# Optimization experiments

Hardware: AMD Instinct MI355X
Metric: run time of the kernel (lower is better)

## Reference

```python
import jax, jax.numpy as jnp
import numpy as np

B, S, D = 32, 1, 2048
H, KVH, HD = 16, 4, 128
MAXS = 4096
EPS = 1e-5
NREP = H // KVH  # GQA repeat factor = 4
FF = 4 * D
POS = 4095  # decode position (start_pos)


def setup_inputs() -> dict:
    key = jax.random.key(0)
    ks = jax.random.split(key, 12)
    sc = lambda d: 1.0 / np.sqrt(d)
    # RoPE angles for the current token position, [S, HD//2]
    inv_freq = 1.0 / (10000.0 ** (np.arange(0, HD, 2, dtype=np.float32) / HD))
    ang = (POS + np.arange(S, dtype=np.float32))[:, None] * inv_freq[None, :]
    return {
        "x": jax.random.normal(ks[0], (B, S, D), jnp.float32),
        "cos": jnp.asarray(np.cos(ang), jnp.float32),
        "sin": jnp.asarray(np.sin(ang), jnp.float32),
        "k_cache": jax.random.normal(ks[1], (B, MAXS, KVH, HD), jnp.float32),
        "v_cache": jax.random.normal(ks[2], (B, MAXS, KVH, HD), jnp.float32),
        "w_rms_attn": jnp.ones((D,), jnp.float32),
        "wq": jax.random.normal(ks[3], (D, D), jnp.float32) * sc(D),
        "wk": jax.random.normal(ks[4], (D, KVH * HD), jnp.float32) * sc(D),
        "wv": jax.random.normal(ks[5], (D, KVH * HD), jnp.float32) * sc(D),
        "wo": jax.random.normal(ks[6], (D, D), jnp.float32) * sc(D),
        "w_rms_ffn": jnp.ones((D,), jnp.float32),
        "w1": jax.random.normal(ks[7], (D, FF), jnp.float32) * sc(D),
        "w2": jax.random.normal(ks[8], (D, FF), jnp.float32) * sc(D),
        "w3": jax.random.normal(ks[9], (FF, D), jnp.float32) * sc(FF),
        "start_pos": POS,
    }


def _rmsnorm(x, g):
    return x * g * jax.lax.rsqrt(jnp.mean(x * x, axis=-1, keepdims=True) + EPS)


def _rope(x, cos, sin):
    # x: [B, S, h, HD]; complex rotation on (even, odd) pairs
    xr = x.reshape(*x.shape[:-1], HD // 2, 2)
    x0, x1 = xr[..., 0], xr[..., 1]
    c = cos[None, :, None, :]
    s = sin[None, :, None, :]
    r0 = x0 * c - x1 * s
    r1 = x0 * s + x1 * c
    return jnp.stack([r0, r1], axis=-1).reshape(x.shape)


def reference(x, cos, sin, k_cache, v_cache, w_rms_attn, wq, wk, wv, wo,
              w_rms_ffn, w1, w2, w3, start_pos):
    xa = _rmsnorm(x, w_rms_attn)
    xq = (xa @ wq).reshape(B, S, H, HD)
    xk = (xa @ wk).reshape(B, S, KVH, HD)
    xv = (xa @ wv).reshape(B, S, KVH, HD)
    # Source applies RoPE to K and V (not Q) -- reproduced faithfully.
    xk = _rope(xk, cos, sin)
    xv = _rope(xv, cos, sin)
    kc = jax.lax.dynamic_update_slice(k_cache, xk, (0, start_pos, 0, 0))
    vc = jax.lax.dynamic_update_slice(v_cache, xv, (0, start_pos, 0, 0))
    klen = start_pos + S
    keys = jnp.repeat(kc[:, :klen], NREP, axis=2)   # [B, klen, H, HD]
    vals = jnp.repeat(vc[:, :klen], NREP, axis=2)
    att = jnp.einsum('bqhd,bkhd->bhqk', xq, keys) * (HD ** -0.5)
    att = jax.nn.softmax(att, axis=-1)
    y = jnp.einsum('bhqk,bkhd->bqhd', att, vals).reshape(B, S, D)
    h = x + y @ wo
    xf = _rmsnorm(h, w_rms_ffn)
    return h + (jax.nn.silu(xf @ w1) * (xf @ w2)) @ w3
```

## Files before the change

kernel.cpp:

```cpp
#include <hip/hip_runtime.h>
#include <math.h>

#define BB 32
#define DD 2048
#define NKVH 4
#define HDIM 128
#define MAXS 4096
#define FFD 8192
#define POS 4095
#define EPSV 1e-5f
#define SCALE 0.08838834764831845f
#define ASPLIT 32
#define SPOS 128

#define OFF_QT   0u
#define OFF_KT   65536u
#define OFF_VT   81920u
#define OFF_G1   98304u
#define OFF_G2   360448u
#define ZERO_N   622592u
#define OFF_XAT  622592u
#define OFF_RK   688128u
#define OFF_RV   704512u
#define OFF_PML  720896u
#define OFF_PACC 753664u
#define OFF_YT   2850816u
#define OFF_H    2916352u
#define OFF_XFT  2981888u
#define OFF_KFIX 3047424u
#define OFF_VFIX 3309568u

#define VM_WAIT8 asm volatile("s_waitcnt vmcnt(8)" ::: "memory")
#define VM_WAIT0 asm volatile("s_waitcnt vmcnt(0)" ::: "memory")
#define LG_WAIT0 asm volatile("s_waitcnt lgkmcnt(0)" ::: "memory")
#define SCHED0   __builtin_amdgcn_sched_barrier(0)
#define SBAR     __builtin_amdgcn_s_barrier()

#define REP32(M) M(0) M(1) M(2) M(3) M(4) M(5) M(6) M(7) M(8) M(9) M(10) M(11) M(12) M(13) M(14) M(15) M(16) M(17) M(18) M(19) M(20) M(21) M(22) M(23) M(24) M(25) M(26) M(27) M(28) M(29) M(30) M(31)
#define REP32A(M,X) M(0,X) M(1,X) M(2,X) M(3,X) M(4,X) M(5,X) M(6,X) M(7,X) M(8,X) M(9,X) M(10,X) M(11,X) M(12,X) M(13,X) M(14,X) M(15,X) M(16,X) M(17,X) M(18,X) M(19,X) M(20,X) M(21,X) M(22,X) M(23,X) M(24,X) M(25,X) M(26,X) M(27,X) M(28,X) M(29,X) M(30,X) M(31,X)

#define DECLA(i) float a##i = 0.f;
#define FMA1(i,k) a##i = fmaf(ap[(k)*32 + (i)], w##k, a##i);
#define STORET(i) tl[i] = a##i;
#define ATOMN(i) atomicAdd(C + (size_t)(i)*N + n, a##i);

template<int N, int CH, bool TOUT>
__device__ __forceinline__ void gemv_body(const float* __restrict__ At,
                                          const float* __restrict__ W,
                                          float* __restrict__ C, int colblk,
                                          float* tile) {
    int tid = (int)threadIdx.x;
    int n = colblk * 256 + tid;
    int d0 = blockIdx.y * CH;
    const float* Wp = W + (size_t)d0 * N + n;
    const float* ap = At + (size_t)d0 * 32;
    REP32(DECLA)
#pragma unroll 4
    for (int dd = 0; dd < CH; dd += 4) {
        float w0 = Wp[0];
        float w1 = Wp[(size_t)N];
        float w2 = Wp[(size_t)N * 2];
        float w3 = Wp[(size_t)N * 3];
        REP32A(FMA1, 0)
        REP32A(FMA1, 1)
        REP32A(FMA1, 2)
        REP32A(FMA1, 3)
        Wp += (size_t)N * 4;
        ap += 128;
    }
    if constexpr (TOUT) {
        float* tl = tile + tid * 33;
        REP32(STORET)
        __syncthreads();
        float* cb = C + (size_t)colblk * 256 * 32;
#pragma unroll
        for (int i = 0; i < 32; ++i) {
            int f = i * 256 + tid;
            atomicAdd(cb + f, tile[(f >> 5) * 33 + (f & 31)]);
        }
    } else {
        REP32(ATOMN)
    }
}

template<int N, int CH, bool TOUT>
__global__ __launch_bounds__(256) void gemv32_kernel(const float* __restrict__ At,
                                                     const float* __restrict__ W,
                                                     float* __restrict__ C) {
    if constexpr (TOUT) {
        __shared__ float tile[256 * 33];
        gemv_body<N, CH, true>(At, W, C, blockIdx.x, tile);
    } else {
        gemv_body<N, CH, false>(At, W, C, blockIdx.x, nullptr);
    }
}

template<int N, int CH, int HALF>
__global__ __launch_bounds__(256) void gemv32_dual_kernel(const float* __restrict__ At,
        const float* __restrict__ W0, const float* __restrict__ W1,
        float* __restrict__ C0, float* __restrict__ C1) {
    __shared__ float tile[256 * 33];
    int bx = blockIdx.x;
    if (bx < HALF) gemv_body<N, CH, true>(At, W0, C0, bx, tile);
    else           gemv_body<N, CH, true>(At, W1, C1, bx - HALF, tile);
}

__global__ void zero_kernel(float* __restrict__ p) {
    p[blockIdx.x * 256 + threadIdx.x] = 0.f;
}

__global__ void rmsnorm_kernel(const float* __restrict__ in, const float* __restrict__ g,
                               float* __restrict__ outT, float* __restrict__ cpy) {
    int b = blockIdx.x;
    int tid = threadIdx.x;
    const float* row = in + b * DD;
    float v[8];
    float ss = 0.f;
#pragma unroll
    for (int i = 0; i < 8; ++i) { v[i] = row[tid + i * 256]; ss += v[i] * v[i]; }
#pragma unroll
    for (int off = 32; off; off >>= 1) ss += __shfl_xor(ss, off);
    __shared__ float red[4];
    if ((tid & 63) == 0) red[tid >> 6] = ss;
    __syncthreads();
    ss = red[0] + red[1] + red[2] + red[3];
    float scale = rsqrtf(ss * (1.f / DD) + EPSV);
#pragma unroll
    for (int i = 0; i < 8; ++i) {
        int idx = tid + i * 256;
        outT[(size_t)idx * 32 + b] = v[i] * g[idx] * scale;
        if (cpy) cpy[b * DD + idx] = v[i];
    }
}

__global__ void rope_kernel(const float* __restrict__ kT, const float* __restrict__ vT,
                            const float* __restrict__ cosb, const float* __restrict__ sinb,
                            float* __restrict__ rk, float* __restrict__ rv) {
    int idx = blockIdx.x * 256 + threadIdx.x;
    int b = idx >> 8, rem = idx & 255;
    int kvh = rem >> 6, i = rem & 63;
    float c = cosb[i], s = sinb[i];
    int col = kvh * HDIM + 2 * i;
    float k0 = kT[(size_t)col * 32 + b], k1 = kT[(size_t)(col + 1) * 32 + b];
    float v0 = vT[(size_t)col * 32 + b], v1 = vT[(size_t)(col + 1) * 32 + b];
    int o = (b * NKVH + kvh) * HDIM + 2 * i;
    rk[o] = k0 * c - k1 * s; rk[o + 1] = k0 * s + k1 * c;
    rv[o] = v0 * c - v1 * s; rv[o + 1] = v0 * s + v1 * c;
}

__global__ void fixlast_kernel(const float* __restrict__ kc, const float* __restrict__ vc,
                               const float* __restrict__ rk, const float* __restrict__ rv,
                               float* __restrict__ kfix, float* __restrict__ vfix) {
    int idx = blockIdx.x * 256 + threadIdx.x;
    int b = idx >> 13, rem = idx & 8191;
    int pos = rem >> 9, col = rem & 511;
    int gpos = 4080 + pos;
    float kv, vv;
    if (gpos == POS) {
        kv = rk[b * 512 + col]; vv = rv[b * 512 + col];
    } else {
        size_t o = ((size_t)(b * MAXS + gpos)) * 512 + col;
        kv = kc[o]; vv = vc[o];
    }
    kfix[idx] = kv; vfix[idx] = vv;
}

__global__ __launch_bounds__(256, 2) void attn_stage_kernel(
    const float* __restrict__ qn, const float* __restrict__ kc, const float* __restrict__ vc,
    const float* __restrict__ kfix, const float* __restrict__ vfix,
    float* __restrict__ pml, float* __restrict__ pacc) {
    int split = blockIdx.x & 31, b = blockIdx.x >> 5;
    int tid = threadIdx.x, lane = tid & 63, wv = tid >> 6;
    __shared__ float kbuf[2][8192];
    __shared__ float p_s[128][16];
    int qpos = tid >> 4, qhead = tid & 15;
    int qr = qpos * 4 + (qhead >> 2);
    int vh = tid >> 4, c16 = tid & 15, vkvh = vh >> 2;
    int t0 = split * SPOS;

    float4 qrot[32];
#pragma unroll
    for (int j = 0; j < 32; ++j) {
        int g = (j + qr) & 31;
        qrot[j] = *(const float4*)(qn + (size_t)b * DD + qhead * HDIM + g * 4);
    }
    float4 av0 = {0, 0, 0, 0}, av1 = {0, 0, 0, 0};

    auto stage = [&](int t) {
        int s = t & 7;
        const float* base;
        if (t < 8) base = (split == 31 && s == 7) ? kfix + (size_t)b * 8192
                                                  : kc + ((size_t)b * MAXS + t0 + s * 16) * 512;
        else       base = (split == 31 && s == 7) ? vfix + (size_t)b * 8192
                                                  : vc + ((size_t)b * MAXS + t0 + s * 16) * 512;
        const float* g = base + wv * 2048 + lane * 4;
        float* l = &kbuf[t & 1][wv * 2048];
#pragma unroll
        for (int i = 0; i < 8; ++i)
            __builtin_amdgcn_global_load_lds(
                (const __attribute__((address_space(1))) void*)(g + i * 256),
                (__attribute__((address_space(3))) void*)(l + i * 256), 16, 0, 0);
    };

    stage(0);
    for (int t = 0; t < 16; ++t) {
        if (t < 15) { stage(t + 1); VM_WAIT8; } else { VM_WAIT0; }
        SCHED0; SBAR;
        if (t == 8) {
#pragma unroll
            for (int hh = 0; hh < 4; ++hh) {
                int h = wv * 4 + hh;
                float e0 = p_s[lane][h], e1 = p_s[lane + 64][h];
                float m = fmaxf(e0, e1);
#pragma unroll
                for (int off = 32; off; off >>= 1) m = fmaxf(m, __shfl_xor(m, off));
                e0 = __expf(e0 - m); e1 = __expf(e1 - m);
                p_s[lane][h] = e0; p_s[lane + 64][h] = e1;
                float l2 = e0 + e1;
#pragma unroll
                for (int off = 32; off; off >>= 1) l2 += __shfl_xor(l2, off);
                if (lane == 0) {
                    int idx = ((b * ASPLIT + split) * 16 + h) * 2;
                    pml[idx] = m; pml[idx + 1] = l2;
                }
            }
        }
        const float* kb = kbuf[t & 1];
        if (t < 8) {
            float4 acc = {0, 0, 0, 0};
            const float* rowp = kb + qr * 128;
#pragma unroll
            for (int j = 0; j < 32; ++j) {
                int g = (j + qr) & 31;
                float4 k4 = *(const float4*)(rowp + g * 4);
                acc.x = fmaf(k4.x, qrot[j].x, acc.x);
                acc.y = fmaf(k4.y, qrot[j].y, acc.y);
                acc.z = fmaf(k4.z, qrot[j].z, acc.z);
                acc.w = fmaf(k4.w, qrot[j].w, acc.w);
            }
            p_s[t * 16 + qpos][qhead] = (acc.x + acc.y + acc.z + acc.w) * SCALE;
        } else {
            int s = t - 8;
            const float* vrow = kb + vkvh * 128 + c16 * 4;
#pragma unroll
            for (int p = 0; p < 16; ++p) {
                float pw = p_s[s * 16 + p][vh];
                float4 v0 = *(const float4*)(vrow + p * 512);
                float4 v1 = *(const float4*)(vrow + p * 512 + 64);
                av0.x = fmaf(pw, v0.x, av0.x); av0.y = fmaf(pw, v0.y, av0.y);
                av0.z = fmaf(pw, v0.z, av0.z); av0.w = fmaf(pw, v0.w, av0.w);
                av1.x = fmaf(pw, v1.x, av1.x); av1.y = fmaf(pw, v1.y, av1.y);
                av1.z = fmaf(pw, v1.z, av1.z); av1.w = fmaf(pw, v1.w, av1.w);
            }
        }
        LG_WAIT0; SCHED0; SBAR;
    }
    size_t pbase = ((size_t)(b * ASPLIT + split) * 16 + vh) * HDIM;
    *(float4*)(pacc + pbase + c16 * 4) = av0;
    *(float4*)(pacc + pbase + 64 + c16 * 4) = av1;
}

__global__ void attn_combine_kernel(const float* __restrict__ pml,
                                    const float* __restrict__ pacc, float* __restrict__ yT) {
    int bid = blockIdx.x;
    int b = bid >> 4, h = bid & 15;
    int d = threadIdx.x;
    float M = -INFINITY;
#pragma unroll 8
    for (int s = 0; s < ASPLIT; ++s)
        M = fmaxf(M, pml[((b * ASPLIT + s) * 16 + h) * 2]);
    float denom = 0.f, acc = 0.f;
#pragma unroll 4
    for (int s = 0; s < ASPLIT; ++s) {
        int idx = (b * ASPLIT + s) * 16 + h;
        float e = __expf(pml[idx * 2] - M);
        denom += pml[idx * 2 + 1] * e;
        acc += e * pacc[(size_t)idx * HDIM + d];
    }
    yT[(size_t)(h * HDIM + d) * 32 + b] = acc / denom;
}

__global__ void silu_mul_kernel(float* __restrict__ g1, const float* __restrict__ g2) {
    int i = blockIdx.x * 256 + threadIdx.x;
    float a = g1[i], bb = g2[i];
    g1[i] = a * bb / (1.f + __expf(-a));
}

extern "C" void kernel_launch(void* const* d_in, const int* in_sizes, int n_in,
                              void* d_out, int out_size, void* d_ws, size_t ws_size,
                              hipStream_t stream) {
    (void)in_sizes; (void)n_in; (void)out_size; (void)ws_size;
    const float* x    = (const float*)d_in[0];
    const float* cosb = (const float*)d_in[1];
    const float* sinb = (const float*)d_in[2];
    const float* kc   = (const float*)d_in[3];
    const float* vc   = (const float*)d_in[4];
    const float* wra  = (const float*)d_in[5];
    const float* wq   = (const float*)d_in[6];
    const float* wk   = (const float*)d_in[7];
    const float* wv   = (const float*)d_in[8];
    const float* wo   = (const float*)d_in[9];
    const float* wrf  = (const float*)d_in[10];
    const float* w1   = (const float*)d_in[11];
    const float* w2   = (const float*)d_in[12];
    const float* w3   = (const float*)d_in[13];
    float* out = (float*)d_out;
    float* ws  = (float*)d_ws;

    float* qn   = ws + OFF_QT;
    float* kT   = ws + OFF_KT;
    float* vT   = ws + OFF_VT;
    float* g1T  = ws + OFF_G1;
    float* g2T  = ws + OFF_G2;
    float* xaT  = ws + OFF_XAT;
    float* rk   = ws + OFF_RK;
    float* rv   = ws + OFF_RV;
    float* pml  = ws + OFF_PML;
    float* pacc = ws + OFF_PACC;
    float* yT   = ws + OFF_YT;
    float* h    = ws + OFF_H;
    float* xfT  = ws + OFF_XFT;
    float* kfix = ws + OFF_KFIX;
    float* vfix = ws + OFF_VFIX;

    zero_kernel<<<ZERO_N / 256, 256, 0, stream>>>(ws);

    rmsnorm_kernel<<<32, 256, 0, stream>>>(x, wra, xaT, h);
    gemv32_kernel<2048, 32, false><<<dim3(8, 64), 256, 0, stream>>>(xaT, wq, qn);
    gemv32_dual_kernel<512, 32, 2><<<dim3(4, 64), 256, 0, stream>>>(xaT, wk, wv, kT, vT);
    rope_kernel<<<32, 256, 0, stream>>>(kT, vT, cosb, sinb, rk, rv);
    fixlast_kernel<<<1024, 256, 0, stream>>>(kc, vc, rk, rv, kfix, vfix);
    attn_stage_kernel<<<1024, 256, 0, stream>>>(qn, kc, vc, kfix, vfix, pml, pacc);
    attn_combine_kernel<<<512, 128, 0, stream>>>(pml, pacc, yT);
    gemv32_kernel<2048, 32, false><<<dim3(8, 64), 256, 0, stream>>>(yT, wo, h);
    rmsnorm_kernel<<<32, 256, 0, stream>>>(h, wrf, xfT, out);
    gemv32_dual_kernel<8192, 128, 32><<<dim3(64, 16), 256, 0, stream>>>(xfT, w1, w2, g1T, g2T);
    silu_mul_kernel<<<1024, 256, 0, stream>>>(g1T, g2T);
    gemv32_kernel<2048, 128, false><<<dim3(8, 64), 256, 0, stream>>>(g1T, w3, out);
}
```

Measured before the change: 309.7 us.

## Make attention waves independent with per-wave buffers and fuse RoPE into fixlast

The attention stage kernel now gives each wavefront its own 32-position slice and its own double-buffered LDS region. Each wave computes a local softmax max and sum, so the block-wide barriers inside the 16-step loop are gone. The four waves' partial results are merged once at the end through LDS with rescaling. The RoPE kernel is folded into the fixlast kernel, which removes one launch and the rk/rv intermediates. The cost is more accumulator registers per thread (8 float4) and an extra intra-block reduction at the end.

Result: no change. 304.2 us (-1.8%).

```diff
diff --git a/kernel.cpp b/kernel.cpp
--- a/kernel.cpp
+++ b/kernel.cpp
@@ -20,8 +20,6 @@
 #define OFF_G2   360448u
 #define ZERO_N   622592u
 #define OFF_XAT  622592u
-#define OFF_RK   688128u
-#define OFF_RV   704512u
 #define OFF_PML  720896u
 #define OFF_PACC 753664u
 #define OFF_YT   2850816u
@@ -30,11 +28,9 @@
 #define OFF_KFIX 3047424u
 #define OFF_VFIX 3309568u
 
-#define VM_WAIT8 asm volatile("s_waitcnt vmcnt(8)" ::: "memory")
-#define VM_WAIT0 asm volatile("s_waitcnt vmcnt(0)" ::: "memory")
-#define LG_WAIT0 asm volatile("s_waitcnt lgkmcnt(0)" ::: "memory")
-#define SCHED0   __builtin_amdgcn_sched_barrier(0)
-#define SBAR     __builtin_amdgcn_s_barrier()
+#define VM_WAIT8  asm volatile("s_waitcnt vmcnt(8)" ::: "memory")
+#define VM_WAIT0  asm volatile("s_waitcnt vmcnt(0)" ::: "memory")
+#define SCHED0    __builtin_amdgcn_sched_barrier(0)
 
 #define REP32(M) M(0) M(1) M(2) M(3) M(4) M(5) M(6) M(7) M(8) M(9) M(10) M(11) M(12) M(13) M(14) M(15) M(16) M(17) M(18) M(19) M(20) M(21) M(22) M(23) M(24) M(25) M(26) M(27) M(28) M(29) M(30) M(31)
 #define REP32A(M,X) M(0,X) M(1,X) M(2,X) M(3,X) M(4,X) M(5,X) M(6,X) M(7,X) M(8,X) M(9,X) M(10,X) M(11,X) M(12,X) M(13,X) M(14,X) M(15,X) M(16,X) M(17,X) M(18,X) M(19,X) M(20,X) M(21,X) M(22,X) M(23,X) M(24,X) M(25,X) M(26,X) M(27,X) M(28,X) M(29,X) M(30,X) M(31,X)
@@ -133,23 +129,9 @@
     }
 }
 
-__global__ void rope_kernel(const float* __restrict__ kT, const float* __restrict__ vT,
-                            const float* __restrict__ cosb, const float* __restrict__ sinb,
-                            float* __restrict__ rk, float* __restrict__ rv) {
-    int idx = blockIdx.x * 256 + threadIdx.x;
-    int b = idx >> 8, rem = idx & 255;
-    int kvh = rem >> 6, i = rem & 63;
-    float c = cosb[i], s = sinb[i];
-    int col = kvh * HDIM + 2 * i;
-    float k0 = kT[(size_t)col * 32 + b], k1 = kT[(size_t)(col + 1) * 32 + b];
-    float v0 = vT[(size_t)col * 32 + b], v1 = vT[(size_t)(col + 1) * 32 + b];
-    int o = (b * NKVH + kvh) * HDIM + 2 * i;
-    rk[o] = k0 * c - k1 * s; rk[o + 1] = k0 * s + k1 * c;
-    rv[o] = v0 * c - v1 * s; rv[o + 1] = v0 * s + v1 * c;
-}
-
-__global__ void fixlast_kernel(const float* __restrict__ kc, const float* __restrict__ vc,
-                               const float* __restrict__ rk, const float* __restrict__ rv,
+__global__ void fixrope_kernel(const float* __restrict__ kc, const float* __restrict__ vc,
+                               const float* __restrict__ kT, const float* __restrict__ vT,
+                               const float* __restrict__ cosb, const float* __restrict__ sinb,
                                float* __restrict__ kfix, float* __restrict__ vfix) {
     int idx = blockIdx.x * 256 + threadIdx.x;
     int b = idx >> 13, rem = idx & 8191;
@@ -157,7 +139,13 @@
     int gpos = 4080 + pos;
     float kv, vv;
     if (gpos == POS) {
-        kv = rk[b * 512 + col]; vv = rv[b * 512 + col];
+        int d = col & 127, i = d >> 1;
+        float c = cosb[i], s = sinb[i];
+        int colp = col & ~1;
+        float k0 = kT[(size_t)colp * 32 + b], k1 = kT[(size_t)(colp + 1) * 32 + b];
+        float v0 = vT[(size_t)colp * 32 + b], v1 = vT[(size_t)(colp + 1) * 32 + b];
+        if (d & 1) { kv = k0 * s + k1 * c; vv = v0 * s + v1 * c; }
+        else       { kv = k0 * c - k1 * s; vv = v0 * c - v1 * s; }
     } else {
         size_t o = ((size_t)(b * MAXS + gpos)) * 512 + col;
         kv = kc[o]; vv = vc[o];
@@ -165,18 +153,20 @@
     kfix[idx] = kv; vfix[idx] = vv;
 }
 
-__global__ __launch_bounds__(256, 2) void attn_stage_kernel(
+__global__ __launch_bounds__(256, 2) void attn_wave_kernel(
     const float* __restrict__ qn, const float* __restrict__ kc, const float* __restrict__ vc,
     const float* __restrict__ kfix, const float* __restrict__ vfix,
     float* __restrict__ pml, float* __restrict__ pacc) {
     int split = blockIdx.x & 31, b = blockIdx.x >> 5;
-    int tid = threadIdx.x, lane = tid & 63, wv = tid >> 6;
-    __shared__ float kbuf[2][8192];
+    int tid = threadIdx.x, w = tid >> 6, lane = tid & 63;
+    __shared__ float kbuf[4][2][2048];
     __shared__ float p_s[128][16];
-    int qpos = tid >> 4, qhead = tid & 15;
-    int qr = qpos * 4 + (qhead >> 2);
-    int vh = tid >> 4, c16 = tid & 15, vkvh = vh >> 2;
+    __shared__ float m_s[4][16], l_s[4][16];
+    int qpos = lane >> 4, qhead = lane & 15;
+    int qr = lane >> 2;
+    int c16 = lane & 15, vh0 = lane >> 4;
     int t0 = split * SPOS;
+    int wbase = w * 32;
 
     float4 qrot[32];
 #pragma unroll
@@ -184,17 +174,21 @@
         int g = (j + qr) & 31;
         qrot[j] = *(const float4*)(qn + (size_t)b * DD + qhead * HDIM + g * 4);
     }
-    float4 av0 = {0, 0, 0, 0}, av1 = {0, 0, 0, 0};
-
-    auto stage = [&](int t) {
-        int s = t & 7;
+    float4 a[8];
+#pragma unroll
+    for (int k = 0; k < 8; ++k) a[k] = (float4){0, 0, 0, 0};
+
+    auto stage = [&](int s) {
+        int sk = s & 7;
+        int g0 = t0 + wbase + sk * 4;
+        bool fix = (split == 31) && (w == 3) && (sk >= 4);
         const float* base;
-        if (t < 8) base = (split == 31 && s == 7) ? kfix + (size_t)b * 8192
-                                                  : kc + ((size_t)b * MAXS + t0 + s * 16) * 512;
-        else       base = (split == 31 && s == 7) ? vfix + (size_t)b * 8192
-                                                  : vc + ((size_t)b * MAXS + t0 + s * 16) * 512;
-        const float* g = base + wv * 2048 + lane * 4;
-        float* l = &kbuf[t & 1][wv * 2048];
+        if (s < 8) base = fix ? kfix + (size_t)b * 8192 + (sk - 4) * 2048
+                              : kc + ((size_t)b * MAXS + g0) * 512;
+        else       base = fix ? vfix + (size_t)b * 8192 + (sk - 4) * 2048
+                              : vc + ((size_t)b * MAXS + g0) * 512;
+        const float* g = base + lane * 4;
+        float* l = &kbuf[w][s & 1][0];
 #pragma unroll
         for (int i = 0; i < 8; ++i)
             __builtin_amdgcn_global_load_lds(
@@ -203,29 +197,11 @@
     };
 
     stage(0);
+#pragma unroll 1
     for (int t = 0; t < 16; ++t) {
         if (t < 15) { stage(t + 1); VM_WAIT8; } else { VM_WAIT0; }
-        SCHED0; SBAR;
-        if (t == 8) {
-#pragma unroll
-            for (int hh = 0; hh < 4; ++hh) {
-                int h = wv * 4 + hh;
-                float e0 = p_s[lane][h], e1 = p_s[lane + 64][h];
-                float m = fmaxf(e0, e1);
-#pragma unroll
-                for (int off = 32; off; off >>= 1) m = fmaxf(m, __shfl_xor(m, off));
-                e0 = __expf(e0 - m); e1 = __expf(e1 - m);
-                p_s[lane][h] = e0; p_s[lane + 64][h] = e1;
-                float l2 = e0 + e1;
-#pragma unroll
-                for (int off = 32; off; off >>= 1) l2 += __shfl_xor(l2, off);
-                if (lane == 0) {
-                    int idx = ((b * ASPLIT + split) * 16 + h) * 2;
-                    pml[idx] = m; pml[idx + 1] = l2;
-                }
-            }
-        }
-        const float* kb = kbuf[t & 1];
+        SCHED0;
+        const float* kb = &kbuf[w][t & 1][0];
         if (t < 8) {
             float4 acc = {0, 0, 0, 0};
             const float* rowp = kb + qr * 128;
@@ -238,26 +214,96 @@
                 acc.z = fmaf(k4.z, qrot[j].z, acc.z);
                 acc.w = fmaf(k4.w, qrot[j].w, acc.w);
             }
-            p_s[t * 16 + qpos][qhead] = (acc.x + acc.y + acc.z + acc.w) * SCALE;
+            p_s[wbase + t * 4 + qpos][qhead] = (acc.x + acc.y + acc.z + acc.w) * SCALE;
+            if (t == 7) {
+                int h = lane >> 2, sub = lane & 3;
+                float v[8];
+                float m = -INFINITY;
+#pragma unroll
+                for (int j = 0; j < 8; ++j) {
+                    v[j] = p_s[wbase + sub * 8 + j][h];
+                    m = fmaxf(m, v[j]);
+                }
+                m = fmaxf(m, __shfl_xor(m, 1));
+                m = fmaxf(m, __shfl_xor(m, 2));
+                float lsum = 0.f;
+#pragma unroll
+                for (int j = 0; j < 8; ++j) {
+                    float e = __expf(v[j] - m);
+                    p_s[wbase + sub * 8 + j][h] = e;
+                    lsum += e;
+                }
+                lsum += __shfl_xor(lsum, 1);
+                lsum += __shfl_xor(lsum, 2);
+                if (sub == 0) { m_s[w][h] = m; l_s[w][h] = lsum; }
+            }
         } else {
             int s = t - 8;
-            const float* vrow = kb + vkvh * 128 + c16 * 4;
-#pragma unroll
-            for (int p = 0; p < 16; ++p) {
-                float pw = p_s[s * 16 + p][vh];
-                float4 v0 = *(const float4*)(vrow + p * 512);
-                float4 v1 = *(const float4*)(vrow + p * 512 + 64);
-                av0.x = fmaf(pw, v0.x, av0.x); av0.y = fmaf(pw, v0.y, av0.y);
-                av0.z = fmaf(pw, v0.z, av0.z); av0.w = fmaf(pw, v0.w, av0.w);
-                av1.x = fmaf(pw, v1.x, av1.x); av1.y = fmaf(pw, v1.y, av1.y);
-                av1.z = fmaf(pw, v1.z, av1.z); av1.w = fmaf(pw, v1.w, av1.w);
+#pragma unroll
+            for (int j = 0; j < 4; ++j) {
+#pragma unroll
+                for (int p = 0; p < 4; ++p) {
+                    float pw = p_s[wbase + s * 4 + p][vh0 + 4 * j];
+                    const float* vr = kb + p * 512 + j * 128 + c16 * 4;
+                    float4 v0 = *(const float4*)(vr);
+                    float4 v1 = *(const float4*)(vr + 64);
+                    a[j * 2].x = fmaf(pw, v0.x, a[j * 2].x);
+                    a[j * 2].y = fmaf(pw, v0.y, a[j * 2].y);
+                    a[j * 2].z = fmaf(pw, v0.z, a[j * 2].z);
+                    a[j * 2].w = fmaf(pw, v0.w, a[j * 2].w);
+                    a[j * 2 + 1].x = fmaf(pw, v1.x, a[j * 2 + 1].x);
+                    a[j * 2 + 1].y = fmaf(pw, v1.y, a[j * 2 + 1].y);
+                    a[j * 2 + 1].z = fmaf(pw, v1.z, a[j * 2 + 1].z);
+                    a[j * 2 + 1].w = fmaf(pw, v1.w, a[j * 2 + 1].w);
+                }
             }
         }
-        LG_WAIT0; SCHED0; SBAR;
-    }
-    size_t pbase = ((size_t)(b * ASPLIT + split) * 16 + vh) * HDIM;
-    *(float4*)(pacc + pbase + c16 * 4) = av0;
-    *(float4*)(pacc + pbase + 64 + c16 * 4) = av1;
+    }
+    __syncthreads();
+    float fac[4];
+#pragma unroll
+    for (int j = 0; j < 4; ++j) {
+        int h = vh0 + 4 * j;
+        float M = fmaxf(fmaxf(m_s[0][h], m_s[1][h]), fmaxf(m_s[2][h], m_s[3][h]));
+        fac[j] = __expf(m_s[w][h] - M);
+    }
+#pragma unroll
+    for (int j = 0; j < 4; ++j) {
+        a[j * 2].x *= fac[j]; a[j * 2].y *= fac[j]; a[j * 2].z *= fac[j]; a[j * 2].w *= fac[j];
+        a[j * 2 + 1].x *= fac[j]; a[j * 2 + 1].y *= fac[j]; a[j * 2 + 1].z *= fac[j]; a[j * 2 + 1].w *= fac[j];
+    }
+    if (w > 0) {
+        float* d = &kbuf[w][0][0];
+#pragma unroll
+        for (int k = 0; k < 8; ++k) *(float4*)(d + lane * 32 + k * 4) = a[k];
+    }
+    __syncthreads();
+    if (w == 0) {
+#pragma unroll
+        for (int wv2 = 1; wv2 < 4; ++wv2) {
+            const float* d = &kbuf[wv2][0][0];
+#pragma unroll
+            for (int k = 0; k < 8; ++k) {
+                float4 t4 = *(const float4*)(d + lane * 32 + k * 4);
+                a[k].x += t4.x; a[k].y += t4.y; a[k].z += t4.z; a[k].w += t4.w;
+            }
+        }
+        size_t pbase = ((size_t)(b * ASPLIT + split) * 16) * HDIM;
+#pragma unroll
+        for (int j = 0; j < 4; ++j) {
+            int h = vh0 + 4 * j;
+            *(float4*)(pacc + pbase + h * HDIM + c16 * 4) = a[j * 2];
+            *(float4*)(pacc + pbase + h * HDIM + 64 + c16 * 4) = a[j * 2 + 1];
+        }
+        if (lane < 16) {
+            int h = lane;
+            float M = fmaxf(fmaxf(m_s[0][h], m_s[1][h]), fmaxf(m_s[2][h], m_s[3][h]));
+            float L = l_s[0][h] * __expf(m_s[0][h] - M) + l_s[1][h] * __expf(m_s[1][h] - M)
+                    + l_s[2][h] * __expf(m_s[2][h] - M) + l_s[3][h] * __expf(m_s[3][h] - M);
+            int idx = ((b * ASPLIT + split) * 16 + h) * 2;
+            pml[idx] = M; pml[idx + 1] = L;
+        }
+    }
 }
 
 __global__ void attn_combine_kernel(const float* __restrict__ pml,
@@ -313,8 +359,6 @@
     float* g1T  = ws + OFF_G1;
     float* g2T  = ws + OFF_G2;
     float* xaT  = ws + OFF_XAT;
-    float* rk   = ws + OFF_RK;
-    float* rv   = ws + OFF_RV;
     float* pml  = ws + OFF_PML;
     float* pacc = ws + OFF_PACC;
     float* yT   = ws + OFF_YT;
@@ -328,9 +372,8 @@
     rmsnorm_kernel<<<32, 256, 0, stream>>>(x, wra, xaT, h);
     gemv32_kernel<2048, 32, false><<<dim3(8, 64), 256, 0, stream>>>(xaT, wq, qn);
     gemv32_dual_kernel<512, 32, 2><<<dim3(4, 64), 256, 0, stream>>>(xaT, wk, wv, kT, vT);
-    rope_kernel<<<32, 256, 0, stream>>>(kT, vT, cosb, sinb, rk, rv);
-    fixlast_kernel<<<1024, 256, 0, stream>>>(kc, vc, rk, rv, kfix, vfix);
-    attn_stage_kernel<<<1024, 256, 0, stream>>>(qn, kc, vc, kfix, vfix, pml, pacc);
+    fixrope_kernel<<<1024, 256, 0, stream>>>(kc, vc, kT, vT, cosb, sinb, kfix, vfix);
+    attn_wave_kernel<<<1024, 256, 0, stream>>>(qn, kc, vc, kfix, vfix, pml, pacc);
     attn_combine_kernel<<<512, 128, 0, stream>>>(pml, pacc, yT);
     gemv32_kernel<2048, 32, false><<<dim3(8, 64), 256, 0, stream>>>(yT, wo, h);
     rmsnorm_kernel<<<32, 256, 0, stream>>>(h, wrf, xfT, out);
```
